# Kernel tuning notes

Hardware: AMD Instinct MI355X
Metric: run time of the kernel (lower is better)

## Reference

```python
import jax, jax.numpy as jnp
import numpy as np

TEMPERATURE = 8.0  # sqrt(head_dim=64)
NEG_BIG = -10000.0


def setup_inputs() -> dict:
    key = jax.random.key(0)
    kq, kk, kv, km = jax.random.split(key, 4)
    B, H, S, D, K = 4, 8, 1024, 64, 4
    q = jax.random.normal(kq, (B, H, S, D), dtype=jnp.float32)
    k = jax.random.normal(kk, (B, H, S, D), dtype=jnp.float32)
    v = jax.random.normal(kv, (B, H, S, D), dtype=jnp.float32)
    # K binary attention masks, broadcastable to [B,H,S,S]
    mask = jax.random.randint(km, (K, 1, 1, S, S), 0, 2).astype(jnp.float32)
    return {"q": q, "k": k, "v": v, "mask": mask}


def reference(q, k, v, mask):
    # attn: [B,H,S,S]
    attn = jnp.einsum("bhsd,bhtd->bhst", q / TEMPERATURE, k)
    # additive mask: [K,1,1,S,S]
    ext_mask = (1.0 - mask) * NEG_BIG
    # batched over K instead of the original python loop: [K,B,H,S,S]
    probs = jax.nn.softmax(attn[None] + ext_mask, axis=-1)
    # dropout is identity in eval mode (deterministic reference)
    output = jnp.einsum("kbhst,bhtd->kbhsd", probs, v)
    return (output, attn)
```

## Files before the change

### kernel.cpp

```cpp
#include <hip/hip_runtime.h>
#include <hip/hip_bf16.h>
#include <stdint.h>

typedef float f4 __attribute__((ext_vector_type(4)));
typedef short bf8 __attribute__((ext_vector_type(8)));
typedef uint32_t u4 __attribute__((ext_vector_type(4)));
typedef uint32_t u2 __attribute__((ext_vector_type(2)));

#define SDIM 1024
#define DDIM 64
#define NBH  32
#define KM   4
#define NT   16

#define MB_BLK 16384
#define KB_BLK 1024
#define VT_BLK 512

__device__ __forceinline__ unsigned short f2bf(float f) {
  uint32_t u = __builtin_bit_cast(uint32_t, f);
  u += 0x7fffu + ((u >> 16) & 1u);
  return (unsigned short)(u >> 16);
}

#define GLOAD16(gsrc, ldst)                                                  \
  __builtin_amdgcn_global_load_lds(                                          \
      (const __attribute__((address_space(1))) unsigned int*)(gsrc),         \
      (__attribute__((address_space(3))) unsigned int*)(ldst), 16, 0, 0)

__device__ __forceinline__ bf8 lds_ld(const unsigned short* base, int row, int e0) {
  return *(const bf8*)((const char*)base + (((row * 64 + e0) * 2) ^ ((row & 7) << 4)));
}

__global__ __launch_bounds__(256) void prepass(
    const float* __restrict__ k, const float* __restrict__ v,
    const float* __restrict__ mask, unsigned short* __restrict__ kb,
    unsigned short* __restrict__ vt, uint32_t* __restrict__ mb2) {
  __shared__ float tv[64][65];
  const int b = blockIdx.x;
  const int t = threadIdx.x;
  if (b < MB_BLK) {
    int gid = b * 256 + t;
    float mv = mask[gid];
    unsigned long long bal = __ballot(mv > 0.5f);
    int lane = t & 63;
    int m = gid >> 20;
    int r = (gid >> 10) & 1023;
    int c = gid & 1023;
    if (lane == 0)       mb2[m * 32768 + (c >> 5) * 1024 + r] = (uint32_t)bal;
    else if (lane == 32) mb2[m * 32768 + (c >> 5) * 1024 + r] = (uint32_t)(bal >> 32);
  } else if (b < MB_BLK + KB_BLK) {
    int base = ((b - MB_BLK) * 256 + t) * 8;
    f4 a = *(const f4*)(k + base);
    f4 c = *(const f4*)(k + base + 4);
    bf8 o;
    o[0] = (short)f2bf(a[0]); o[1] = (short)f2bf(a[1]);
    o[2] = (short)f2bf(a[2]); o[3] = (short)f2bf(a[3]);
    o[4] = (short)f2bf(c[0]); o[5] = (short)f2bf(c[1]);
    o[6] = (short)f2bf(c[2]); o[7] = (short)f2bf(c[3]);
    *(bf8*)(kb + base) = o;
  } else {
    int vb = b - MB_BLK - KB_BLK;
    int bh = vb >> 4;
    int s0 = (vb & 15) * 64;
    int sr = t >> 2, c0 = (t & 3) * 16;
    const float* vp = v + ((size_t)(bh * SDIM) + s0 + sr) * DDIM + c0;
#pragma unroll
    for (int i = 0; i < 4; ++i) {
      f4 x = *(const f4*)(vp + 4 * i);
#pragma unroll
      for (int j = 0; j < 4; ++j) tv[sr][c0 + 4 * i + j] = x[j];
    }
    __syncthreads();
    int d = t >> 2, sc0 = (t & 3) * 16;
    unsigned short tmp[16];
#pragma unroll
    for (int i = 0; i < 16; ++i) tmp[i] = f2bf(tv[sc0 + i][d]);
    unsigned short* op = vt + ((size_t)(bh * DDIM) + d) * SDIM + s0 + sc0;
    bf8 o0, o1;
#pragma unroll
    for (int j = 0; j < 8; ++j) { o0[j] = (short)tmp[j]; o1[j] = (short)tmp[j + 8]; }
    *(bf8*)(op) = o0;
    *(bf8*)(op + 8) = o1;
  }
}

__global__ __launch_bounds__(256, 4) void attn_main(
    const float* __restrict__ qf, const unsigned short* __restrict__ kb,
    const unsigned short* __restrict__ vtg, const uint32_t* __restrict__ mb2,
    float* __restrict__ outO, float* __restrict__ attn) {
  __shared__ __align__(16) unsigned short k_s0[64 * 64];
  __shared__ __align__(16) unsigned short k_s1[64 * 64];
  __shared__ __align__(16) unsigned short v_s0[64 * 64];
  __shared__ __align__(16) unsigned short v_s1[64 * 64];
  __shared__ __align__(16) unsigned short e_s[32 * 64];

  const int tid = threadIdx.x;
  const int l   = tid & 63;
  const int w   = tid >> 6;
  const int l16 = l & 15;
  const int lg  = l >> 4;
  const int wh  = w & 1;
  const int wc  = w >> 1;

  int bid = (int)blockIdx.x;
  bid = (bid & 7) * 128 + (bid >> 3);
  const int bh = bid >> 5;
  const int r0 = (bid & 31) * 32;

  const int srow = tid >> 3;
  const int sd   = ((tid & 7) ^ (srow & 7)) << 3;
  const unsigned short* ksrc0 = kb  + ((size_t)(bh * SDIM) + srow) * DDIM + sd;
  const unsigned short* ksrc1 = kb  + ((size_t)(bh * SDIM) + srow + 32) * DDIM + sd;
  const unsigned short* vsrc0 = vtg + ((size_t)(bh * DDIM) + srow) * SDIM + sd;
  const unsigned short* vsrc1 = vtg + ((size_t)(bh * DDIM) + srow + 32) * SDIM + sd;

  GLOAD16(ksrc0, k_s0 + tid * 8);
  GLOAD16(ksrc1, k_s0 + (tid + 256) * 8);
  GLOAD16(vsrc0, v_s0 + tid * 8);
  GLOAD16(vsrc1, v_s0 + (tid + 256) * 8);

  bf8 bq0, bq1;
  {
    const float* qp = qf + ((size_t)(bh * SDIM) + r0 + 16 * wh + l16) * DDIM + lg * 8;
    f4 a0 = *(const f4*)qp;
    f4 a1 = *(const f4*)(qp + 4);
    f4 a2 = *(const f4*)(qp + 32);
    f4 a3 = *(const f4*)(qp + 36);
#pragma unroll
    for (int j = 0; j < 4; ++j) {
      bq0[j]     = (short)f2bf(a0[j] * 0.125f);
      bq0[j + 4] = (short)f2bf(a1[j] * 0.125f);
      bq1[j]     = (short)f2bf(a2[j] * 0.125f);
      bq1[j + 4] = (short)f2bf(a3[j] * 0.125f);
    }
  }

  f4 acc[2][4] = {};
  f4 accl[2]   = {};
  bf8 ones;
#pragma unroll
  for (int b = 0; b < 8; ++b) ones[b] = (short)0x3F80;

  const uint32_t* mbase = mb2 + w * 32768 + r0 + l16;

  uint32_t mdwA[2][2], mdwB[2][2];
#pragma unroll
  for (int mt2 = 0; mt2 < 2; ++mt2)
#pragma unroll
    for (int kt = 0; kt < 2; ++kt)
      mdwA[mt2][kt] = mbase[kt * 1024 + 16 * mt2];

  __syncthreads();

#define BODY(CT, KR, VR, KW, VW, MR, MW, PF)                                   \
  {                                                                            \
    if (PF) {                                                                  \
      GLOAD16(ksrc0 + (size_t)((CT) + 1) * 4096, (KW) + tid * 8);              \
      GLOAD16(ksrc1 + (size_t)((CT) + 1) * 4096, (KW) + (tid + 256) * 8);      \
      GLOAD16(vsrc0 + (size_t)((CT) + 1) * 64, (VW) + tid * 8);                \
      GLOAD16(vsrc1 + (size_t)((CT) + 1) * 64, (VW) + (tid + 256) * 8);        \
    }                                                                          \
    {                                                                          \
      const int kc0 = 32 * wc + l16;                                           \
      bf8 ak0 = lds_ld((KR), kc0, lg * 8);                                     \
      bf8 ak1 = lds_ld((KR), kc0, lg * 8 + 32);                                \
      bf8 ak2 = lds_ld((KR), kc0 + 16, lg * 8);                                \
      bf8 ak3 = lds_ld((KR), kc0 + 16, lg * 8 + 32);                           \
      f4 s0 = {}, s1 = {};                                                     \
      s0 = __builtin_amdgcn_mfma_f32_16x16x32_bf16(ak0, bq0, s0, 0, 0, 0);     \
      s0 = __builtin_amdgcn_mfma_f32_16x16x32_bf16(ak1, bq1, s0, 0, 0, 0);     \
      s1 = __builtin_amdgcn_mfma_f32_16x16x32_bf16(ak2, bq0, s1, 0, 0, 0);     \
      s1 = __builtin_amdgcn_mfma_f32_16x16x32_bf16(ak3, bq1, s1, 0, 0, 0);     \
      float* arow = attn + ((size_t)(bh * SDIM) + r0 + 16 * wh + l16) * SDIM   \
                    + (CT) * 64 + 32 * wc + 4 * lg;                            \
      *(f4*)(arow) = s0;                                                       \
      *(f4*)(arow + 16) = s1;                                                  \
      const int erow = 16 * wh + l16;                                          \
      u2 ev0, ev1;                                                             \
      ev0[0] = (uint32_t)f2bf(__expf(s0[0])) | ((uint32_t)f2bf(__expf(s0[1])) << 16); \
      ev0[1] = (uint32_t)f2bf(__expf(s0[2])) | ((uint32_t)f2bf(__expf(s0[3])) << 16); \
      ev1[0] = (uint32_t)f2bf(__expf(s1[0])) | ((uint32_t)f2bf(__expf(s1[1])) << 16); \
      ev1[1] = (uint32_t)f2bf(__expf(s1[2])) | ((uint32_t)f2bf(__expf(s1[3])) << 16); \
      const int colA = 32 * wc + 4 * lg;                                       \
      *(u2*)((char*)e_s + (((erow * 64 + colA) * 2) ^ ((erow & 7) << 4))) = ev0; \
      *(u2*)((char*)e_s + (((erow * 64 + colA + 16) * 2) ^ ((erow & 7) << 4))) = ev1; \
    }                                                                          \
    asm volatile("s_waitcnt lgkmcnt(0)\n\ts_barrier" ::: "memory");            \
    {                                                                          \
      bf8 af[2][2];                                                            \
      _Pragma("unroll") for (int mt2 = 0; mt2 < 2; ++mt2) {                    \
        const int row = 16 * mt2 + l16;                                        \
        _Pragma("unroll") for (int kt = 0; kt < 2; ++kt) {                     \
          bf8 e = lds_ld(e_s, row, kt * 32 + lg * 8);                          \
          uint32_t bits = ((MR)[mt2][kt] >> (lg * 8)) & 0xffu;                 \
          u4 ew = __builtin_bit_cast(u4, e);                                   \
          _Pragma("unroll") for (int d = 0; d < 4; ++d) {                      \
            uint32_t n2 = (bits >> (2 * d)) & 3u;                              \
            uint32_t sp = (n2 * 0x8001u) & 0x00010001u;                        \
            ew[d] &= (sp << 16) - sp;                                          \
          }                                                                    \
          af[mt2][kt] = __builtin_bit_cast(bf8, ew);                           \
        }                                                                      \
      }                                                                        \
      __builtin_amdgcn_s_setprio(1);                                           \
      _Pragma("unroll") for (int mt2 = 0; mt2 < 2; ++mt2) {                    \
        accl[mt2] = __builtin_amdgcn_mfma_f32_16x16x32_bf16(af[mt2][0], ones, accl[mt2], 0, 0, 0); \
        accl[mt2] = __builtin_amdgcn_mfma_f32_16x16x32_bf16(af[mt2][1], ones, accl[mt2], 0, 0, 0); \
      }                                                                        \
      _Pragma("unroll") for (int nt = 0; nt < 4; ++nt) {                       \
        const int dc = 16 * nt + l16;                                          \
        bf8 bv0 = lds_ld((VR), dc, lg * 8);                                    \
        bf8 bv1 = lds_ld((VR), dc, lg * 8 + 32);                               \
        _Pragma("unroll") for (int mt2 = 0; mt2 < 2; ++mt2) {                  \
          acc[mt2][nt] = __builtin_amdgcn_mfma_f32_16x16x32_bf16(af[mt2][0], bv0, acc[mt2][nt], 0, 0, 0); \
          acc[mt2][nt] = __builtin_amdgcn_mfma_f32_16x16x32_bf16(af[mt2][1], bv1, acc[mt2][nt], 0, 0, 0); \
        }                                                                      \
      }                                                                        \
      __builtin_amdgcn_s_setprio(0);                                           \
    }                                                                          \
    if (PF) {                                                                  \
      _Pragma("unroll") for (int mt2 = 0; mt2 < 2; ++mt2)                      \
        _Pragma("unroll") for (int kt = 0; kt < 2; ++kt)                       \
          (MW)[mt2][kt] = mbase[(((CT) + 1) * 2 + kt) * 1024 + 16 * mt2];      \
    }                                                                          \
    __syncthreads();                                                           \
  }

  for (int ct2 = 0; ct2 < NT / 2; ++ct2) {
    BODY(2 * ct2,     k_s0, v_s0, k_s1, v_s1, mdwA, mdwB, true);
    BODY(2 * ct2 + 1, k_s1, v_s1, k_s0, v_s0, mdwB, mdwA, (ct2 < NT / 2 - 1));
  }
#undef BODY

#pragma unroll
  for (int mt2 = 0; mt2 < 2; ++mt2) {
#pragma unroll
    for (int r = 0; r < 4; ++r) {
      float inv = 1.0f / accl[mt2][r];
      int row = 16 * mt2 + 4 * lg + r;
      float* orow = outO + (((size_t)(w * NBH + bh)) * SDIM + r0 + row) * DDIM + l16;
#pragma unroll
      for (int nt = 0; nt < 4; ++nt)
        orow[16 * nt] = acc[mt2][nt][r] * inv;
    }
  }
}

extern "C" void kernel_launch(void* const* d_in, const int* in_sizes, int n_in,
                              void* d_out, int out_size, void* d_ws, size_t ws_size,
                              hipStream_t stream) {
  (void)in_sizes; (void)n_in; (void)out_size; (void)ws_size;
  const float* q    = (const float*)d_in[0];
  const float* k    = (const float*)d_in[1];
  const float* v    = (const float*)d_in[2];
  const float* mask = (const float*)d_in[3];
  float* outO = (float*)d_out;
  float* attn = (float*)d_out + (size_t)KM * NBH * SDIM * DDIM;

  char* ws = (char*)d_ws;
  unsigned short* kb = (unsigned short*)ws;
  unsigned short* vt = (unsigned short*)(ws + (4u << 20));
  uint32_t*       mb = (uint32_t*)(ws + (8u << 20));

  prepass<<<MB_BLK + KB_BLK + VT_BLK, 256, 0, stream>>>(k, v, mask, kb, vt, mb);
  attn_main<<<NBH * 32, 256, 0, stream>>>(q, kb, vt, mb, outO, attn);
}
```

Measured before the change: 57.34 us.

## Vectorize mask bit-packing, use nontemporal stores, drop setprio around MFMA

The mask prepass now loads four floats per thread and builds each 32-bit mask word with lane shuffles instead of a one-float-per-thread ballot, so it launches a quarter as many blocks. The attn and output stores become nontemporal to limit cache pollution from the large write-only outputs. The s_setprio raise around the MFMA section is removed, and the ones-vector MFMAs are merged into the mask-building loop. The stores change cache behaviour, and dropping the priority hint may shift how waves interleave.

```diff
diff --git a/kernel.cpp b/kernel.cpp
--- a/kernel.cpp
+++ b/kernel.cpp
@@ -13,7 +13,7 @@
 #define KM   4
 #define NT   16
 
-#define MB_BLK 16384
+#define MB_BLK 4096
 #define KB_BLK 1024
 #define VT_BLK 512
 
@@ -40,15 +40,20 @@
   const int b = blockIdx.x;
   const int t = threadIdx.x;
   if (b < MB_BLK) {
-    int gid = b * 256 + t;
-    float mv = mask[gid];
-    unsigned long long bal = __ballot(mv > 0.5f);
-    int lane = t & 63;
-    int m = gid >> 20;
-    int r = (gid >> 10) & 1023;
-    int c = gid & 1023;
-    if (lane == 0)       mb2[m * 32768 + (c >> 5) * 1024 + r] = (uint32_t)bal;
-    else if (lane == 32) mb2[m * 32768 + (c >> 5) * 1024 + r] = (uint32_t)(bal >> 32);
+    int gid4 = (b * 256 + t) * 4;
+    f4 x = *(const f4*)(mask + gid4);
+    uint32_t bits = (x[0] > 0.5f ? 1u : 0u) | (x[1] > 0.5f ? 2u : 0u) |
+                    (x[2] > 0.5f ? 4u : 0u) | (x[3] > 0.5f ? 8u : 0u);
+    uint32_t wv = bits << (gid4 & 28);
+    wv |= __shfl_xor(wv, 1);
+    wv |= __shfl_xor(wv, 2);
+    wv |= __shfl_xor(wv, 4);
+    if ((t & 7) == 0) {
+      int m = gid4 >> 20;
+      int r = (gid4 >> 10) & 1023;
+      int c = gid4 & 1023;
+      mb2[m * 32768 + (c >> 5) * 1024 + r] = wv;
+    }
   } else if (b < MB_BLK + KB_BLK) {
     int base = ((b - MB_BLK) * 256 + t) * 8;
     f4 a = *(const f4*)(k + base);
@@ -174,8 +179,8 @@
       s1 = __builtin_amdgcn_mfma_f32_16x16x32_bf16(ak3, bq1, s1, 0, 0, 0);     \
       float* arow = attn + ((size_t)(bh * SDIM) + r0 + 16 * wh + l16) * SDIM   \
                     + (CT) * 64 + 32 * wc + 4 * lg;                            \
-      *(f4*)(arow) = s0;                                                       \
-      *(f4*)(arow + 16) = s1;                                                  \
+      __builtin_nontemporal_store(s0, (f4*)arow);                              \
+      __builtin_nontemporal_store(s1, (f4*)(arow + 16));                       \
       const int erow = 16 * wh + l16;                                          \
       u2 ev0, ev1;                                                             \
       ev0[0] = (uint32_t)f2bf(__expf(s0[0])) | ((uint32_t)f2bf(__expf(s0[1])) << 16); \
@@ -202,9 +207,6 @@
           }                                                                    \
           af[mt2][kt] = __builtin_bit_cast(bf8, ew);                           \
         }                                                                      \
-      }                                                                        \
-      __builtin_amdgcn_s_setprio(1);                                           \
-      _Pragma("unroll") for (int mt2 = 0; mt2 < 2; ++mt2) {                    \
         accl[mt2] = __builtin_amdgcn_mfma_f32_16x16x32_bf16(af[mt2][0], ones, accl[mt2], 0, 0, 0); \
         accl[mt2] = __builtin_amdgcn_mfma_f32_16x16x32_bf16(af[mt2][1], ones, accl[mt2], 0, 0, 0); \
       }                                                                        \
@@ -217,7 +219,6 @@
           acc[mt2][nt] = __builtin_amdgcn_mfma_f32_16x16x32_bf16(af[mt2][1], bv1, acc[mt2][nt], 0, 0, 0); \
         }                                                                      \
       }                                                                        \
-      __builtin_amdgcn_s_setprio(0);                                           \
     }                                                                          \
     if (PF) {                                                                  \
       _Pragma("unroll") for (int mt2 = 0; mt2 < 2; ++mt2)                      \
@@ -242,7 +243,7 @@
       float* orow = outO + (((size_t)(w * NBH + bh)) * SDIM + r0 + row) * DDIM + l16;
 #pragma unroll
       for (int nt = 0; nt < 4; ++nt)
-        orow[16 * nt] = acc[mt2][nt][r] * inv;
+        __builtin_nontemporal_store(acc[mt2][nt][r] * inv, orow + 16 * nt);
     }
   }
 }
```

Result: slower. 74.98 us (+30.8%).
